# Kernel tuning notes

Measured on AMD Instinct MI355X. Metric: run time of the kernel, lower is better.

Reference implementation:

```python
import jax, jax.numpy as jnp
import numpy as np

K = 32        # neighbors per anchor (cfg.k)
LN_EPS = 1e-6 # flax LayerNorm default


def _layer_norm(x, g, b):
    mu = jnp.mean(x, axis=-1, keepdims=True)
    var = jnp.var(x, axis=-1, keepdims=True)
    return (x - mu) * jax.lax.rsqrt(var + LN_EPS) * g + b


def setup_inputs() -> dict:
    key = jax.random.key(0)
    ks = jax.random.split(key, 8)
    b, n, m, c = 4, 8192, 2048, 64
    feats, hidden = 128, 64  # cfg.features, cfg.features // 2
    cin = 3 + c              # delta_coord (3) concat neighbor feats (c)
    feat = jax.random.normal(ks[0], (b, n, c), jnp.float32)
    coord = jax.random.uniform(ks[1], (b, n, 3), jnp.float32)
    anchor_feat = jax.random.normal(ks[2], (b, m, c), jnp.float32)
    anchor_coord = jax.random.uniform(ks[3], (b, m, 3), jnp.float32)
    W1 = jax.random.normal(ks[4], (cin, hidden), jnp.float32) / np.sqrt(cin).astype(np.float32)
    b1 = jnp.zeros((hidden,), jnp.float32)
    g1 = jnp.ones((hidden,), jnp.float32)
    be1 = jnp.zeros((hidden,), jnp.float32)
    W2 = jax.random.normal(ks[5], (hidden, feats), jnp.float32) / np.sqrt(hidden).astype(np.float32)
    b2 = jnp.zeros((feats,), jnp.float32)
    g2 = jnp.ones((feats,), jnp.float32)
    be2 = jnp.zeros((feats,), jnp.float32)
    return dict(feat=feat, coord=coord, anchor_feat=anchor_feat,
                anchor_coord=anchor_coord, W1=W1, b1=b1, g1=g1, be1=be1,
                W2=W2, b2=b2, g2=g2, be2=be2)


def reference(feat, coord, anchor_feat, anchor_coord,
              W1, b1, g1, be1, W2, b2, g2, be2):
    # --- kNN: squared distances [b, m, n], take K smallest ---
    d2 = (jnp.sum(anchor_coord ** 2, axis=-1)[..., None]
          - 2.0 * jnp.einsum('bmd,bnd->bmn', anchor_coord, coord)
          + jnp.sum(coord ** 2, axis=-1)[:, None, :])
    _, idx = jax.lax.top_k(-d2, K)  # idx: [b, m, K]

    gather = jax.vmap(lambda arr, i: arr[i])  # batch_lookup
    k_feat = gather(feat, idx) - anchor_feat[..., None, :]   # [b,m,K,c] (anchor_feat_offset)
    k_coord = gather(coord, idx)                             # [b,m,K,3]

    delta = k_coord - anchor_coord[..., None, :]             # [b,m,K,3]
    norms = jnp.linalg.norm(delta, axis=-1, keepdims=True)   # [b,m,K,1]
    delta = delta / jnp.max(norms, axis=(-1, -2, -3), keepdims=True)  # per-batch max norm

    x = jnp.concatenate([delta, k_feat], axis=-1)            # [b,m,K,3+c]
    # GroupMLP: Dense -> LN -> relu, Dense -> LN -> relu, max pool over K
    x = jax.nn.relu(_layer_norm(x @ W1 + b1, g1, be1))
    x = jax.nn.relu(_layer_norm(x @ W2 + b2, g2, be2))
    return jnp.max(x, axis=-2)                               # [b, m, features]
```

## Files before the change

kernel.cpp:

```cpp
#include <hip/hip_runtime.h>
#include <math.h>

#define BB 4
#define NN 8192
#define MM 2048
#define CC 64
#define KNB 32
#define CIN 67
#define H1 64
#define H2 128
#define XP 36
#define AB 4

__global__ void init_kernel(int* maxnorm) {
    if (threadIdx.x < BB) maxnorm[threadIdx.x] = 0;
}

__global__ __launch_bounds__(256) void coord4_kernel(const float* __restrict__ coord,
                                                     float4* __restrict__ c4) {
    const int t = blockIdx.x * 256 + threadIdx.x;
    if (t < BB * NN) {
        float cx = coord[t * 3 + 0], cy = coord[t * 3 + 1], cz = coord[t * 3 + 2];
        float c2 = __fadd_rn(__fadd_rn(__fmul_rn(cx, cx), __fmul_rn(cy, cy)), __fmul_rn(cz, cz));
        float4 q; q.x = cx; q.y = cy; q.z = cz; q.w = c2;
        c4[t] = q;
    }
}

__global__ __launch_bounds__(256, 4) void knn_kernel(
    const float4* __restrict__ c4buf, const float* __restrict__ anchor_coord,
    int* __restrict__ idxbuf, int* __restrict__ maxnorm)
{
    __shared__ unsigned hist[4][256];
    __shared__ unsigned wmax[4];
    __shared__ unsigned wtot[4];
    __shared__ unsigned bc[2];
    __shared__ unsigned nsel;
    __shared__ int      selcell;
    __shared__ int      sel_s[KNB];

    const int anchor = blockIdx.x;
    const int b  = anchor >> 11;
    const int mi = anchor & (MM - 1);
    const int tid = threadIdx.x;
    const int w = tid >> 6, lane = tid & 63;

    const float ax = anchor_coord[(b * MM + mi) * 3 + 0];
    const float ay = anchor_coord[(b * MM + mi) * 3 + 1];
    const float az = anchor_coord[(b * MM + mi) * 3 + 2];
    const float a2 = __fadd_rn(__fadd_rn(__fmul_rn(ax, ax), __fmul_rn(ay, ay)), __fmul_rn(az, az));

    const float4* c4b = c4buf + (size_t)b * NN;

    unsigned kreg[32];
    unsigned tmin = 0xFFFFFFFFu;
    #pragma unroll
    for (int j = 0; j < 32; j++) {
        const int i = tid + 256 * j;
        const float4 cq = c4b[i];
        float dt = __fadd_rn(__fadd_rn(__fmul_rn(ax, cq.x), __fmul_rn(ay, cq.y)), __fmul_rn(az, cq.z));
        float d2 = __fadd_rn(__fsub_rn(a2, __fmul_rn(2.0f, dt)), cq.w);
        unsigned ub = __float_as_uint(d2);
        ub ^= (unsigned)((int)ub >> 31) | 0x80000000u;
        kreg[j] = ub;
        tmin = tmin < ub ? tmin : ub;
    }

    unsigned um = tmin;
    um = max(um, (unsigned)__shfl_xor((int)um, 1));
    um = max(um, (unsigned)__shfl_xor((int)um, 2));
    um = max(um, (unsigned)__shfl_xor((int)um, 4));
    if (lane == 0) wmax[w] = um;
    if (tid == 0) nsel = 0;
    __syncthreads();
    const unsigned U = max(max(wmax[0], wmax[1]), max(wmax[2], wmax[3]));

    unsigned prefix = 0, pmask = 0;
    unsigned k = KNB;

    #pragma unroll
    for (int pass = 0; pass < 4; pass++) {
        const int sh = 24 - 8 * pass;
        unsigned* hf = &hist[0][0];
        hf[tid] = 0; hf[tid + 256] = 0; hf[tid + 512] = 0; hf[tid + 768] = 0;
        __syncthreads();
        #pragma unroll
        for (int j = 0; j < 32; j++) {
            unsigned kk = kreg[j];
            if (kk <= U && (kk & pmask) == prefix) atomicAdd(&hist[w][(kk >> sh) & 0xFFu], 1u);
        }
        __syncthreads();
        const unsigned h = hist[0][tid] + hist[1][tid] + hist[2][tid] + hist[3][tid];
        unsigned v = h;
        #pragma unroll
        for (int d = 1; d < 64; d <<= 1) {
            unsigned t = __shfl_up(v, d);
            if (lane >= d) v += t;
        }
        if (lane == 63) wtot[w] = v;
        __syncthreads();
        unsigned off = 0;
        #pragma unroll
        for (int ww = 0; ww < 3; ww++) if (ww < w) off += wtot[ww];
        v += off;
        const unsigned excl = v - h;
        if (excl < k && k <= v) { bc[0] = (unsigned)tid; bc[1] = k - excl; }
        __syncthreads();
        prefix |= bc[0] << sh;
        pmask  |= 0xFFu << sh;
        k = bc[1];
    }
    const unsigned T = prefix;

    unsigned tiemask = 0;
    #pragma unroll
    for (int j = 0; j < 32; j++) {
        unsigned kk = kreg[j];
        if (kk < T) { unsigned pos = atomicAdd(&nsel, 1u); sel_s[pos] = tid + 256 * j; }
        else if (kk == T) tiemask |= 1u << j;
    }
    __syncthreads();
    const unsigned n_lt = nsel;
    const unsigned needed = KNB - n_lt;
    int last = -1;
    for (unsigned r = 0; r < needed; r++) {
        if (tid == 0) selcell = 0x7fffffff;
        __syncthreads();
        unsigned m = tiemask;
        while (m) {
            int j = __ffs(m) - 1; m &= m - 1;
            int idx = tid + 256 * j;
            if (idx > last) atomicMin(&selcell, idx);
        }
        __syncthreads();
        last = selcell;
        if (tid == 0) sel_s[n_lt + r] = last;
        __syncthreads();
    }

    float nrm = 0.0f;
    if (tid < KNB) {
        int j = sel_s[tid];
        idxbuf[anchor * KNB + tid] = j;
        const float4 cq = c4b[j];
        float dx = __fsub_rn(cq.x, ax);
        float dy = __fsub_rn(cq.y, ay);
        float dz = __fsub_rn(cq.z, az);
        nrm = sqrtf(dx * dx + dy * dy + dz * dz);
    }
    if (tid < 64) {
        #pragma unroll
        for (int off = 32; off; off >>= 1) nrm = fmaxf(nrm, __shfl_xor(nrm, off));
        if (tid == 0) atomicMax(&maxnorm[b], __float_as_int(nrm));
    }
}

__global__ __launch_bounds__(256, 4) void mlp_kernel(
    const float* __restrict__ feat, const float* __restrict__ coord,
    const float* __restrict__ anchor_feat, const float* __restrict__ anchor_coord,
    const float* __restrict__ W1, const float* __restrict__ b1,
    const float* __restrict__ g1, const float* __restrict__ be1,
    const float* __restrict__ W2, const float* __restrict__ b2,
    const float* __restrict__ g2, const float* __restrict__ be2,
    const int* __restrict__ maxnorm, const int* __restrict__ idxbuf,
    float* __restrict__ out)
{
    __shared__ __align__(16) float xst[AB][CIN * XP];
    __shared__ int sel[AB][KNB];

    const int a0g = blockIdx.x * AB;
    const int b   = a0g >> 11;
    const int tid = threadIdx.x;
    const int w = tid >> 6, lane = tid & 63;
    const int g = tid >> 5, c = tid & 31;

    if (tid < AB * KNB) sel[tid >> 5][tid & 31] = idxbuf[(size_t)a0g * KNB + tid];
    __syncthreads();

    const float mn = __int_as_float(maxnorm[b]);

    {
        const int mi = (a0g + w) & (MM - 1);
        const float af = anchor_feat[((size_t)b * MM + mi) * CC + lane];
        #pragma unroll 8
        for (int kk = 0; kk < KNB; kk++) {
            const int nj = sel[w][kk];
            xst[w][(3 + lane) * XP + kk] = feat[((size_t)b * NN + nj) * CC + lane] - af;
        }
    }
    for (int t = tid; t < AB * KNB * 3; t += 256) {
        const int a = t / 96, r = t % 96, k = r / 3, j = r % 3;
        const int mi = (a0g + a) & (MM - 1);
        const int nj = sel[a][k];
        float d = __fsub_rn(coord[((size_t)b * NN + nj) * 3 + j],
                            anchor_coord[((size_t)b * MM + mi) * 3 + j]);
        xst[a][j * XP + k] = __fdiv_rn(d, mn);
    }
    __syncthreads();

    const int ch1 = 2 * c;
    const float b1a = b1[ch1], b1b = b1[ch1 + 1];
    float accA[AB][4], accB[AB][4];
    #pragma unroll
    for (int a = 0; a < AB; a++)
        #pragma unroll
        for (int kk = 0; kk < 4; kk++) { accA[a][kk] = b1a; accB[a][kk] = b1b; }
    #pragma unroll 4
    for (int j = 0; j < CIN; j++) {
        const float2 wv = *(const float2*)&W1[j * H1 + ch1];
        #pragma unroll
        for (int a = 0; a < AB; a++) {
            const float4 xq = *(const float4*)&xst[a][j * XP + 4 * g];
            accA[a][0] = fmaf(xq.x, wv.x, accA[a][0]);  accB[a][0] = fmaf(xq.x, wv.y, accB[a][0]);
            accA[a][1] = fmaf(xq.y, wv.x, accA[a][1]);  accB[a][1] = fmaf(xq.y, wv.y, accB[a][1]);
            accA[a][2] = fmaf(xq.z, wv.x, accA[a][2]);  accB[a][2] = fmaf(xq.z, wv.y, accB[a][2]);
            accA[a][3] = fmaf(xq.w, wv.x, accA[a][3]);  accB[a][3] = fmaf(xq.w, wv.y, accB[a][3]);
        }
    }
    const float g1a = g1[ch1], g1b = g1[ch1 + 1];
    const float be1a = be1[ch1], be1b = be1[ch1 + 1];
    float y1A[AB][4], y1B[AB][4];
    #pragma unroll
    for (int a = 0; a < AB; a++) {
        #pragma unroll
        for (int kk = 0; kk < 4; kk++) {
            float s  = accA[a][kk] + accB[a][kk];
            float s2 = accA[a][kk] * accA[a][kk] + accB[a][kk] * accB[a][kk];
            #pragma unroll
            for (int off = 16; off; off >>= 1) { s += __shfl_xor(s, off); s2 += __shfl_xor(s2, off); }
            float mu  = s  * (1.0f / H1);
            float var = s2 * (1.0f / H1) - mu * mu;
            float r = rsqrtf(var + 1e-6f);
            y1A[a][kk] = fmaxf(fmaf((accA[a][kk] - mu) * r, g1a, be1a), 0.0f);
            y1B[a][kk] = fmaxf(fmaf((accB[a][kk] - mu) * r, g1b, be1b), 0.0f);
        }
    }
    __syncthreads();
    #pragma unroll
    for (int a = 0; a < AB; a++)
        #pragma unroll
        for (int kk = 0; kk < 4; kk++) {
            xst[a][ch1 * XP + 4 * g + kk]       = y1A[a][kk];
            xst[a][(ch1 + 1) * XP + 4 * g + kk] = y1B[a][kk];
        }
    __syncthreads();

    const int ch2 = 4 * c;
    const float4 b2v = *(const float4*)&b2[ch2];
    float a2c[AB][16];
    #pragma unroll
    for (int a = 0; a < AB; a++)
        #pragma unroll
        for (int kk = 0; kk < 4; kk++) {
            a2c[a][0 * 4 + kk] = b2v.x; a2c[a][1 * 4 + kk] = b2v.y;
            a2c[a][2 * 4 + kk] = b2v.z; a2c[a][3 * 4 + kk] = b2v.w;
        }
    #pragma unroll 2
    for (int j = 0; j < H1; j++) {
        const float4 wv = *(const float4*)&W2[j * H2 + ch2];
        #pragma unroll
        for (int a = 0; a < AB; a++) {
            const float4 hq = *(const float4*)&xst[a][j * XP + 4 * g];
            a2c[a][0]  = fmaf(hq.x, wv.x, a2c[a][0]);  a2c[a][1]  = fmaf(hq.y, wv.x, a2c[a][1]);
            a2c[a][2]  = fmaf(hq.z, wv.x, a2c[a][2]);  a2c[a][3]  = fmaf(hq.w, wv.x, a2c[a][3]);
            a2c[a][4]  = fmaf(hq.x, wv.y, a2c[a][4]);  a2c[a][5]  = fmaf(hq.y, wv.y, a2c[a][5]);
            a2c[a][6]  = fmaf(hq.z, wv.y, a2c[a][6]);  a2c[a][7]  = fmaf(hq.w, wv.y, a2c[a][7]);
            a2c[a][8]  = fmaf(hq.x, wv.z, a2c[a][8]);  a2c[a][9]  = fmaf(hq.y, wv.z, a2c[a][9]);
            a2c[a][10] = fmaf(hq.z, wv.z, a2c[a][10]); a2c[a][11] = fmaf(hq.w, wv.z, a2c[a][11]);
            a2c[a][12] = fmaf(hq.x, wv.w, a2c[a][12]); a2c[a][13] = fmaf(hq.y, wv.w, a2c[a][13]);
            a2c[a][14] = fmaf(hq.z, wv.w, a2c[a][14]); a2c[a][15] = fmaf(hq.w, wv.w, a2c[a][15]);
        }
    }
    const float4 g2v  = *(const float4*)&g2[ch2];
    const float4 be2v = *(const float4*)&be2[ch2];
    float mx[AB][4];
    #pragma unroll
    for (int a = 0; a < AB; a++) {
        mx[a][0] = -INFINITY; mx[a][1] = -INFINITY; mx[a][2] = -INFINITY; mx[a][3] = -INFINITY;
        #pragma unroll
        for (int kk = 0; kk < 4; kk++) {
            float v0 = a2c[a][kk], v1 = a2c[a][4 + kk], v2 = a2c[a][8 + kk], v3 = a2c[a][12 + kk];
            float s  = (v0 + v1) + (v2 + v3);
            float s2 = (v0 * v0 + v1 * v1) + (v2 * v2 + v3 * v3);
            #pragma unroll
            for (int off = 16; off; off >>= 1) { s += __shfl_xor(s, off); s2 += __shfl_xor(s2, off); }
            float mu  = s  * (1.0f / H2);
            float var = s2 * (1.0f / H2) - mu * mu;
            float r = rsqrtf(var + 1e-6f);
            mx[a][0] = fmaxf(mx[a][0], fmaxf(fmaf((v0 - mu) * r, g2v.x, be2v.x), 0.0f));
            mx[a][1] = fmaxf(mx[a][1], fmaxf(fmaf((v1 - mu) * r, g2v.y, be2v.y), 0.0f));
            mx[a][2] = fmaxf(mx[a][2], fmaxf(fmaf((v2 - mu) * r, g2v.z, be2v.z), 0.0f));
            mx[a][3] = fmaxf(mx[a][3], fmaxf(fmaf((v3 - mu) * r, g2v.w, be2v.w), 0.0f));
        }
    }
    __syncthreads();
    float* pmaxp = &xst[0][0];
    #pragma unroll
    for (int a = 0; a < AB; a++) {
        float4 q; q.x = mx[a][0]; q.y = mx[a][1]; q.z = mx[a][2]; q.w = mx[a][3];
        *(float4*)&pmaxp[(a * 8 + g) * H2 + ch2] = q;
    }
    __syncthreads();
    #pragma unroll
    for (int t = tid; t < AB * H2; t += 256) {
        const int a = t >> 7, ch = t & 127;
        float vv = pmaxp[(a * 8 + 0) * H2 + ch];
        #pragma unroll
        for (int gg = 1; gg < 8; gg++) vv = fmaxf(vv, pmaxp[(a * 8 + gg) * H2 + ch]);
        out[(size_t)(a0g + a) * H2 + ch] = vv;
    }
}

extern "C" void kernel_launch(void* const* d_in, const int* in_sizes, int n_in,
                              void* d_out, int out_size, void* d_ws, size_t ws_size,
                              hipStream_t stream) {
    const float* feat         = (const float*)d_in[0];
    const float* coord        = (const float*)d_in[1];
    const float* anchor_feat  = (const float*)d_in[2];
    const float* anchor_coord = (const float*)d_in[3];
    const float* W1  = (const float*)d_in[4];
    const float* b1  = (const float*)d_in[5];
    const float* g1  = (const float*)d_in[6];
    const float* be1 = (const float*)d_in[7];
    const float* W2  = (const float*)d_in[8];
    const float* b2  = (const float*)d_in[9];
    const float* g2  = (const float*)d_in[10];
    const float* be2 = (const float*)d_in[11];
    float* out = (float*)d_out;

    int*    maxn   = (int*)d_ws;
    int*    idxbuf = (int*)d_ws + 16;
    float4* c4buf  = (float4*)((int*)d_ws + 16 + BB * MM * KNB);

    init_kernel<<<1, 64, 0, stream>>>(maxn);
    coord4_kernel<<<(BB * NN + 255) / 256, 256, 0, stream>>>(coord, c4buf);
    knn_kernel<<<BB * MM, 256, 0, stream>>>(c4buf, anchor_coord, idxbuf, maxn);
    mlp_kernel<<<BB * MM / AB, 256, 0, stream>>>(feat, coord, anchor_feat, anchor_coord,
                                                 W1, b1, g1, be1, W2, b2, g2, be2,
                                                 maxn, idxbuf, out);
}
```

Measured before the change: 228.3 us.

## Process two anchors per kNN block to share coordinate loads and barriers

Each kNN block now handles two anchors, so every coordinate float4 it loads is used for two distance computations, and the radix-select passes run both histograms under the same barriers. This halves the number of blocks and the global coordinate traffic per anchor, and amortises the synchronisation cost. In exchange it doubles the per-thread key registers (64 instead of 32) and the shared histogram size, which may lower occupancy under the 256x4 launch bound or cause register spills. Pass 0 also drops the redundant prefix check.

```diff
diff --git a/kernel.cpp b/kernel.cpp
--- a/kernel.cpp
+++ b/kernel.cpp
@@ -31,118 +31,171 @@
     const float4* __restrict__ c4buf, const float* __restrict__ anchor_coord,
     int* __restrict__ idxbuf, int* __restrict__ maxnorm)
 {
-    __shared__ unsigned hist[4][256];
-    __shared__ unsigned wmax[4];
-    __shared__ unsigned wtot[4];
-    __shared__ unsigned bc[2];
-    __shared__ unsigned nsel;
-    __shared__ int      selcell;
-    __shared__ int      sel_s[KNB];
-
-    const int anchor = blockIdx.x;
-    const int b  = anchor >> 11;
-    const int mi = anchor & (MM - 1);
+    __shared__ unsigned hist[2][4][256];
+    __shared__ unsigned wmax[2][4];
+    __shared__ unsigned wtot[2][4];
+    __shared__ unsigned bc[2][2];
+    __shared__ unsigned nsel[2];
+    __shared__ int      selcell[2];
+    __shared__ int      sel_s[2][KNB];
+
+    const int a0 = blockIdx.x * 2;
+    const int b  = a0 >> 11;
+    const int mi = a0 & (MM - 1);
     const int tid = threadIdx.x;
     const int w = tid >> 6, lane = tid & 63;
 
-    const float ax = anchor_coord[(b * MM + mi) * 3 + 0];
-    const float ay = anchor_coord[(b * MM + mi) * 3 + 1];
-    const float az = anchor_coord[(b * MM + mi) * 3 + 2];
-    const float a2 = __fadd_rn(__fadd_rn(__fmul_rn(ax, ax), __fmul_rn(ay, ay)), __fmul_rn(az, az));
+    const float axA = anchor_coord[(b * MM + mi) * 3 + 0];
+    const float ayA = anchor_coord[(b * MM + mi) * 3 + 1];
+    const float azA = anchor_coord[(b * MM + mi) * 3 + 2];
+    const float a2A = __fadd_rn(__fadd_rn(__fmul_rn(axA, axA), __fmul_rn(ayA, ayA)), __fmul_rn(azA, azA));
+    const float axB = anchor_coord[(b * MM + mi + 1) * 3 + 0];
+    const float ayB = anchor_coord[(b * MM + mi + 1) * 3 + 1];
+    const float azB = anchor_coord[(b * MM + mi + 1) * 3 + 2];
+    const float a2B = __fadd_rn(__fadd_rn(__fmul_rn(axB, axB), __fmul_rn(ayB, ayB)), __fmul_rn(azB, azB));
 
     const float4* c4b = c4buf + (size_t)b * NN;
 
-    unsigned kreg[32];
-    unsigned tmin = 0xFFFFFFFFu;
+    unsigned kregA[32], kregB[32];
+    unsigned tminA = 0xFFFFFFFFu, tminB = 0xFFFFFFFFu;
     #pragma unroll
     for (int j = 0; j < 32; j++) {
         const int i = tid + 256 * j;
         const float4 cq = c4b[i];
-        float dt = __fadd_rn(__fadd_rn(__fmul_rn(ax, cq.x), __fmul_rn(ay, cq.y)), __fmul_rn(az, cq.z));
-        float d2 = __fadd_rn(__fsub_rn(a2, __fmul_rn(2.0f, dt)), cq.w);
-        unsigned ub = __float_as_uint(d2);
-        ub ^= (unsigned)((int)ub >> 31) | 0x80000000u;
-        kreg[j] = ub;
-        tmin = tmin < ub ? tmin : ub;
-    }
-
-    unsigned um = tmin;
-    um = max(um, (unsigned)__shfl_xor((int)um, 1));
-    um = max(um, (unsigned)__shfl_xor((int)um, 2));
-    um = max(um, (unsigned)__shfl_xor((int)um, 4));
-    if (lane == 0) wmax[w] = um;
-    if (tid == 0) nsel = 0;
-    __syncthreads();
-    const unsigned U = max(max(wmax[0], wmax[1]), max(wmax[2], wmax[3]));
-
-    unsigned prefix = 0, pmask = 0;
-    unsigned k = KNB;
+        float dtA = __fadd_rn(__fadd_rn(__fmul_rn(axA, cq.x), __fmul_rn(ayA, cq.y)), __fmul_rn(azA, cq.z));
+        float d2A = __fadd_rn(__fsub_rn(a2A, __fmul_rn(2.0f, dtA)), cq.w);
+        unsigned ubA = __float_as_uint(d2A);
+        ubA ^= (unsigned)((int)ubA >> 31) | 0x80000000u;
+        kregA[j] = ubA;
+        tminA = tminA < ubA ? tminA : ubA;
+        float dtB = __fadd_rn(__fadd_rn(__fmul_rn(axB, cq.x), __fmul_rn(ayB, cq.y)), __fmul_rn(azB, cq.z));
+        float d2B = __fadd_rn(__fsub_rn(a2B, __fmul_rn(2.0f, dtB)), cq.w);
+        unsigned ubB = __float_as_uint(d2B);
+        ubB ^= (unsigned)((int)ubB >> 31) | 0x80000000u;
+        kregB[j] = ubB;
+        tminB = tminB < ubB ? tminB : ubB;
+    }
+
+    unsigned umA = tminA, umB = tminB;
+    umA = max(umA, (unsigned)__shfl_xor((int)umA, 1));
+    umA = max(umA, (unsigned)__shfl_xor((int)umA, 2));
+    umA = max(umA, (unsigned)__shfl_xor((int)umA, 4));
+    umB = max(umB, (unsigned)__shfl_xor((int)umB, 1));
+    umB = max(umB, (unsigned)__shfl_xor((int)umB, 2));
+    umB = max(umB, (unsigned)__shfl_xor((int)umB, 4));
+    if (lane == 0) { wmax[0][w] = umA; wmax[1][w] = umB; }
+    if (tid == 0) { nsel[0] = 0; nsel[1] = 0; }
+    __syncthreads();
+    const unsigned UA = max(max(wmax[0][0], wmax[0][1]), max(wmax[0][2], wmax[0][3]));
+    const unsigned UB = max(max(wmax[1][0], wmax[1][1]), max(wmax[1][2], wmax[1][3]));
+
+    unsigned prefA = 0, prefB = 0, pmask = 0;
+    unsigned kA = KNB, kB = KNB;
 
     #pragma unroll
     for (int pass = 0; pass < 4; pass++) {
         const int sh = 24 - 8 * pass;
-        unsigned* hf = &hist[0][0];
-        hf[tid] = 0; hf[tid + 256] = 0; hf[tid + 512] = 0; hf[tid + 768] = 0;
+        unsigned* hf = &hist[0][0][0];
+        #pragma unroll
+        for (int q = 0; q < 8; q++) hf[tid + 256 * q] = 0;
         __syncthreads();
-        #pragma unroll
-        for (int j = 0; j < 32; j++) {
-            unsigned kk = kreg[j];
-            if (kk <= U && (kk & pmask) == prefix) atomicAdd(&hist[w][(kk >> sh) & 0xFFu], 1u);
+        if (pass == 0) {
+            #pragma unroll
+            for (int j = 0; j < 32; j++) {
+                if (kregA[j] <= UA) atomicAdd(&hist[0][w][kregA[j] >> 24], 1u);
+                if (kregB[j] <= UB) atomicAdd(&hist[1][w][kregB[j] >> 24], 1u);
+            }
+        } else {
+            #pragma unroll
+            for (int j = 0; j < 32; j++) {
+                if ((kregA[j] & pmask) == prefA) atomicAdd(&hist[0][w][(kregA[j] >> sh) & 0xFFu], 1u);
+                if ((kregB[j] & pmask) == prefB) atomicAdd(&hist[1][w][(kregB[j] >> sh) & 0xFFu], 1u);
+            }
         }
         __syncthreads();
-        const unsigned h = hist[0][tid] + hist[1][tid] + hist[2][tid] + hist[3][tid];
-        unsigned v = h;
+        const unsigned hA = hist[0][0][tid] + hist[0][1][tid] + hist[0][2][tid] + hist[0][3][tid];
+        const unsigned hB = hist[1][0][tid] + hist[1][1][tid] + hist[1][2][tid] + hist[1][3][tid];
+        unsigned vA = hA, vB = hB;
         #pragma unroll
         for (int d = 1; d < 64; d <<= 1) {
-            unsigned t = __shfl_up(v, d);
-            if (lane >= d) v += t;
-        }
-        if (lane == 63) wtot[w] = v;
+            unsigned tA = __shfl_up(vA, d);
+            unsigned tB = __shfl_up(vB, d);
+            if (lane >= d) { vA += tA; vB += tB; }
+        }
+        if (lane == 63) { wtot[0][w] = vA; wtot[1][w] = vB; }
         __syncthreads();
-        unsigned off = 0;
-        #pragma unroll
-        for (int ww = 0; ww < 3; ww++) if (ww < w) off += wtot[ww];
-        v += off;
-        const unsigned excl = v - h;
-        if (excl < k && k <= v) { bc[0] = (unsigned)tid; bc[1] = k - excl; }
+        unsigned offA = 0, offB = 0;
+        #pragma unroll
+        for (int ww = 0; ww < 3; ww++) if (ww < w) { offA += wtot[0][ww]; offB += wtot[1][ww]; }
+        vA += offA; vB += offB;
+        const unsigned exclA = vA - hA, exclB = vB - hB;
+        if (exclA < kA && kA <= vA) { bc[0][0] = (unsigned)tid; bc[0][1] = kA - exclA; }
+        if (exclB < kB && kB <= vB) { bc[1][0] = (unsigned)tid; bc[1][1] = kB - exclB; }
         __syncthreads();
-        prefix |= bc[0] << sh;
-        pmask  |= 0xFFu << sh;
-        k = bc[1];
-    }
-    const unsigned T = prefix;
-
-    unsigned tiemask = 0;
+        prefA |= bc[0][0] << sh; kA = bc[0][1];
+        prefB |= bc[1][0] << sh; kB = bc[1][1];
+        pmask |= 0xFFu << sh;
+    }
+    const unsigned TA = prefA, TB = prefB;
+
+    unsigned tiemaskA = 0, tiemaskB = 0;
     #pragma unroll
     for (int j = 0; j < 32; j++) {
-        unsigned kk = kreg[j];
-        if (kk < T) { unsigned pos = atomicAdd(&nsel, 1u); sel_s[pos] = tid + 256 * j; }
-        else if (kk == T) tiemask |= 1u << j;
-    }
-    __syncthreads();
-    const unsigned n_lt = nsel;
-    const unsigned needed = KNB - n_lt;
-    int last = -1;
-    for (unsigned r = 0; r < needed; r++) {
-        if (tid == 0) selcell = 0x7fffffff;
-        __syncthreads();
-        unsigned m = tiemask;
-        while (m) {
-            int j = __ffs(m) - 1; m &= m - 1;
-            int idx = tid + 256 * j;
-            if (idx > last) atomicMin(&selcell, idx);
-        }
-        __syncthreads();
-        last = selcell;
-        if (tid == 0) sel_s[n_lt + r] = last;
-        __syncthreads();
+        unsigned kkA = kregA[j];
+        if (kkA < TA) { unsigned p = atomicAdd(&nsel[0], 1u); sel_s[0][p] = tid + 256 * j; }
+        else if (kkA == TA) tiemaskA |= 1u << j;
+        unsigned kkB = kregB[j];
+        if (kkB < TB) { unsigned p = atomicAdd(&nsel[1], 1u); sel_s[1][p] = tid + 256 * j; }
+        else if (kkB == TB) tiemaskB |= 1u << j;
+    }
+    __syncthreads();
+    {
+        const unsigned n_lt = nsel[0];
+        const unsigned needed = KNB - n_lt;
+        int last = -1;
+        for (unsigned r = 0; r < needed; r++) {
+            if (tid == 0) selcell[0] = 0x7fffffff;
+            __syncthreads();
+            unsigned m = tiemaskA;
+            while (m) {
+                int j = __ffs(m) - 1; m &= m - 1;
+                int idx = tid + 256 * j;
+                if (idx > last) atomicMin(&selcell[0], idx);
+            }
+            __syncthreads();
+            last = selcell[0];
+            if (tid == 0) sel_s[0][n_lt + r] = last;
+            __syncthreads();
+        }
+    }
+    {
+        const unsigned n_lt = nsel[1];
+        const unsigned needed = KNB - n_lt;
+        int last = -1;
+        for (unsigned r = 0; r < needed; r++) {
+            if (tid == 0) selcell[1] = 0x7fffffff;
+            __syncthreads();
+            unsigned m = tiemaskB;
+            while (m) {
+                int j = __ffs(m) - 1; m &= m - 1;
+                int idx = tid + 256 * j;
+                if (idx > last) atomicMin(&selcell[1], idx);
+            }
+            __syncthreads();
+            last = selcell[1];
+            if (tid == 0) sel_s[1][n_lt + r] = last;
+            __syncthreads();
+        }
     }
 
     float nrm = 0.0f;
-    if (tid < KNB) {
-        int j = sel_s[tid];
-        idxbuf[anchor * KNB + tid] = j;
+    if (tid < 64) {
+        const int a = tid >> 5;
+        const int s = tid & 31;
+        const int j = sel_s[a][s];
+        idxbuf[(size_t)(a0 + a) * KNB + s] = j;
         const float4 cq = c4b[j];
+        const float ax = a ? axB : axA, ay = a ? ayB : ayA, az = a ? azB : azA;
         float dx = __fsub_rn(cq.x, ax);
         float dy = __fsub_rn(cq.y, ay);
         float dz = __fsub_rn(cq.z, az);
@@ -334,7 +387,7 @@
 
     init_kernel<<<1, 64, 0, stream>>>(maxn);
     coord4_kernel<<<(BB * NN + 255) / 256, 256, 0, stream>>>(coord, c4buf);
-    knn_kernel<<<BB * MM, 256, 0, stream>>>(c4buf, anchor_coord, idxbuf, maxn);
+    knn_kernel<<<BB * MM / 2, 256, 0, stream>>>(c4buf, anchor_coord, idxbuf, maxn);
     mlp_kernel<<<BB * MM / AB, 256, 0, stream>>>(feat, coord, anchor_feat, anchor_coord,
                                                  W1, b1, g1, be1, W2, b2, g2, be2,
                                                  maxn, idxbuf, out);
```

Result: faster. 204.9 us, median of 3 (-10.2%).
